# Performance work log

Hardware: AMD Instinct MI355X
Metric: run time of the kernel (lower is better)

Reference implementation:

```python
import jax, jax.numpy as jnp
import numpy as np

B, S, E, H, DH = 4, 2048, 1024, 16, 64  # batch, seq, embed, heads, head_dim


def setup_inputs() -> dict:
    key = jax.random.key(0)
    k0, k1, k2, k3 = jax.random.split(key, 4)
    scale = 1.0 / np.sqrt(E).astype(np.float32)
    embedded = jax.random.normal(k0, (B, S, E), jnp.float32)
    Wq = jax.random.normal(k1, (H, E, DH), jnp.float32) * scale
    Wk = jax.random.normal(k2, (H, E, DH), jnp.float32) * scale
    Wv = jax.random.normal(k3, (H, E, DH), jnp.float32) * scale
    return {"embedded": embedded, "Wq": Wq, "Wk": Wk, "Wv": Wv}


def reference(embedded, Wq, Wk, Wv):
    # Batched QKV projections across all heads (replaces per-head nn.Linear loop)
    q = jnp.einsum('bse,hed->bhsd', embedded, Wq)
    k = jnp.einsum('bse,hed->bhsd', embedded, Wk)
    v = jnp.einsum('bse,hed->bhsd', embedded, Wv)
    head_dim = q.shape[-1]
    scores = jnp.einsum('bhqd,bhkd->bhqk', q, k) / jnp.sqrt(jnp.asarray(head_dim, q.dtype))
    seq = scores.shape[-1]
    causal = jnp.tril(jnp.ones((seq, seq), dtype=bool))  # lower-triangular causal mask
    scores = jnp.where(causal, scores, jnp.finfo(scores.dtype).min)
    attn = jax.nn.softmax(scores, axis=-1)
    out = jnp.einsum('bhqk,bhkd->bhqd', attn, v)
    # concatenate heads along the feature dim (torch.cat(..., dim=2))
    b, h, s, d = out.shape
    return out.transpose(0, 2, 1, 3).reshape(b, s, h * d)
```

## Files before the change

### kernel.cpp

```cpp
#include <hip/hip_runtime.h>


typedef short bf16x4 __attribute__((ext_vector_type(4)));
typedef short bf16x8 __attribute__((ext_vector_type(8)));
typedef float f32x4 __attribute__((ext_vector_type(4)));
typedef unsigned short u16x4 __attribute__((ext_vector_type(4)));
typedef unsigned short u16x8 __attribute__((ext_vector_type(8)));

#define SCL 0.1803368801111204f

static __device__ __forceinline__ unsigned short f2bf(float f) {
  unsigned int u = __builtin_bit_cast(unsigned int, f);
  u += 0x7fffu + ((u >> 16) & 1u);
  return (unsigned short)(u >> 16);
}

static __device__ __forceinline__ void gload16(const void* g, void* l) {
  __builtin_amdgcn_global_load_lds((__attribute__((address_space(1))) void*)g,
                                   (__attribute__((address_space(3))) void*)l, 16, 0, 0);
}

__global__ __launch_bounds__(256) void conv_x(const float* __restrict__ x,
                                              unsigned short* __restrict__ y, int n4) {
  int i0 = blockIdx.x * 256 + threadIdx.x;
  int stride = gridDim.x * 256;
  for (int c = i0; c < n4; c += stride) {
    float4 v = ((const float4*)x)[c];
    u16x4 o;
    o[0] = f2bf(v.x); o[1] = f2bf(v.y); o[2] = f2bf(v.z); o[3] = f2bf(v.w);
    ((u16x4*)y)[c] = o;
  }
}

__global__ __launch_bounds__(256) void conv_w(const float* __restrict__ Wq,
                                              const float* __restrict__ Wk,
                                              const float* __restrict__ Wv,
                                              unsigned short* __restrict__ Wt) {
  const int p = blockIdx.y;
  const float* Wsrc = (p == 0) ? Wq : ((p == 1) ? Wk : Wv);
  const int h = blockIdx.x >> 4, et = blockIdx.x & 15;
  const int t = threadIdx.x;
  __shared__ __align__(16) unsigned short tile[64][72];

  const float* src = Wsrc + (h * 1024 + et * 64) * 64;
#pragma unroll
  for (int i = 0; i < 4; ++i) {
    int c = i * 256 + t;
    int r = c >> 4, cc = (c & 15) * 4;
    float4 v = *(const float4*)(src + r * 64 + cc);
    tile[r][cc + 0] = f2bf(v.x); tile[r][cc + 1] = f2bf(v.y);
    tile[r][cc + 2] = f2bf(v.z); tile[r][cc + 3] = f2bf(v.w);
  }
  __syncthreads();
#pragma unroll
  for (int i = 0; i < 2; ++i) {
    int c = i * 256 + t;
    int d = c >> 3, ec = (c & 7) * 8;
    u16x8 o;
#pragma unroll
    for (int j = 0; j < 8; ++j) o[j] = tile[ec + j][d];
    *(u16x8*)(Wt + (p * 1024 + h * 64 + d) * 1024 + et * 64 + ec) = o;
  }
}

__global__ __launch_bounds__(512, 2) void qkv_gemm(const unsigned short* __restrict__ Xb,
                                                   const unsigned short* __restrict__ Wt,
                                                   unsigned short* __restrict__ Qb,
                                                   unsigned short* __restrict__ Kb,
                                                   unsigned short* __restrict__ Vtb) {
  __shared__ __align__(16) unsigned short L[3][2][256 * 32];

  const int t = threadIdx.x, lane = t & 63, w = t >> 6;
  const int wr = w >> 2, wc = w & 3, c16 = lane & 15, g = lane >> 4;

  const int bid = blockIdx.x;
  const int xcd = bid & 7, l = bid >> 3;
  const int nt = l >> 2;
  const int m0 = (xcd * 4 + (l & 3)) * 256;
  const int p = nt >> 2;
  const int nb0 = (nt & 3) * 256;

  f32x4 acc[8][4] = {};

  const int srow = t >> 2;
  const int scl = (t & 3) ^ ((srow & 3) ^ ((srow >> 2) & 3));
  const int chp = (g ^ ((c16 & 3) ^ ((c16 >> 2) & 3))) * 8;

#define STAGE(KT, AB, HALF, BUF)                                                   \
  {                                                                                \
    const unsigned short* s_ =                                                     \
        (((AB) == 0) ? (Xb + (m0 + (HALF)*128) * 1024)                             \
                     : (Wt + (p * 1024 + nb0 + (HALF)*128) * 1024)) +              \
        (KT)*32 + srow * 1024 + scl * 8;                                           \
    gload16(s_, &L[BUF][AB][(HALF)*4096 + w * 512]);                               \
  }
#define LDA(BUF, MI) (*(const bf16x8*)&L[BUF][0][(wr * 128 + (MI)*16 + c16) * 32 + chp])
#define LDB(BUF, NI) (*(const bf16x8*)&L[BUF][1][(wc * 64 + (NI)*16 + c16) * 32 + chp])

  STAGE(0, 0, 0, 0); STAGE(0, 0, 1, 0); STAGE(0, 1, 0, 0); STAGE(0, 1, 1, 0);
  STAGE(1, 0, 0, 1); STAGE(1, 0, 1, 1); STAGE(1, 1, 0, 1); STAGE(1, 1, 1, 1);

  int buf = 0;
#pragma unroll 1
  for (int kt = 0; kt < 32; ++kt) {
    const int sbuf = (buf == 0) ? 2 : buf - 1;
    if (kt < 31) { asm volatile("s_waitcnt vmcnt(4)" ::: "memory"); }
    else         { asm volatile("s_waitcnt vmcnt(0)" ::: "memory"); }
    __builtin_amdgcn_s_barrier();

    bf16x8 bq[4], aq[4];
#pragma unroll
    for (int ni = 0; ni < 4; ++ni) bq[ni] = LDB(buf, ni);
#pragma unroll
    for (int mi = 0; mi < 4; ++mi) aq[mi] = LDA(buf, mi);
    if (kt < 30) { STAGE(kt + 2, 0, 0, sbuf); STAGE(kt + 2, 0, 1, sbuf); }
    asm volatile("s_waitcnt lgkmcnt(0)" ::: "memory");
    __builtin_amdgcn_sched_barrier(0);
    __builtin_amdgcn_s_setprio(1);
    if (p != 2) {
#pragma unroll
      for (int q = 0; q < 4; ++q)
#pragma unroll
        for (int ni = 0; ni < 4; ++ni)
          acc[q][ni] = __builtin_amdgcn_mfma_f32_16x16x32_bf16(aq[q], bq[ni], acc[q][ni], 0, 0, 0);
    } else {
#pragma unroll
      for (int q = 0; q < 4; ++q)
#pragma unroll
        for (int ni = 0; ni < 4; ++ni)
          acc[q][ni] = __builtin_amdgcn_mfma_f32_16x16x32_bf16(bq[ni], aq[q], acc[q][ni], 0, 0, 0);
    }
    __builtin_amdgcn_s_setprio(0);

    bf16x8 aq2[4];
#pragma unroll
    for (int mi = 0; mi < 4; ++mi) aq2[mi] = LDA(buf, 4 + mi);
    if (kt < 30) { STAGE(kt + 2, 1, 0, sbuf); STAGE(kt + 2, 1, 1, sbuf); }
    asm volatile("s_waitcnt lgkmcnt(0)" ::: "memory");
    __builtin_amdgcn_sched_barrier(0);
    __builtin_amdgcn_s_setprio(1);
    if (p != 2) {
#pragma unroll
      for (int q = 0; q < 4; ++q)
#pragma unroll
        for (int ni = 0; ni < 4; ++ni)
          acc[4 + q][ni] = __builtin_amdgcn_mfma_f32_16x16x32_bf16(aq2[q], bq[ni], acc[4 + q][ni], 0, 0, 0);
    } else {
#pragma unroll
      for (int q = 0; q < 4; ++q)
#pragma unroll
        for (int ni = 0; ni < 4; ++ni)
          acc[4 + q][ni] = __builtin_amdgcn_mfma_f32_16x16x32_bf16(bq[ni], aq2[q], acc[4 + q][ni], 0, 0, 0);
    }
    __builtin_amdgcn_s_setprio(0);

    buf = (buf == 2) ? 0 : buf + 1;
  }

  if (p != 2) {
    unsigned short* dst = (p == 0) ? Qb : Kb;
#pragma unroll
    for (int mi = 0; mi < 8; ++mi)
#pragma unroll
      for (int ni = 0; ni < 4; ++ni)
#pragma unroll
        for (int r = 0; r < 4; ++r) {
          int m_g = m0 + wr * 128 + mi * 16 + g * 4 + r;
          int n_g = nb0 + wc * 64 + ni * 16 + c16;
          int b = m_g >> 11, s = m_g & 2047;
          dst[((b * 16 + (n_g >> 6)) * 2048 + s) * 64 + (n_g & 63)] = f2bf(acc[mi][ni][r]);
        }
  } else {
#pragma unroll
    for (int mi = 0; mi < 8; ++mi)
#pragma unroll
      for (int ni = 0; ni < 4; ++ni)
#pragma unroll
        for (int r = 0; r < 4; ++r) {
          int n_g = nb0 + wc * 64 + ni * 16 + g * 4 + r;
          int m_g = m0 + wr * 128 + mi * 16 + c16;
          int b = m_g >> 11, s = m_g & 2047;
          Vtb[((b * 16 + (n_g >> 6)) * 64 + (n_g & 63)) * 2048 + s] = f2bf(acc[mi][ni][r]);
        }
  }
#undef STAGE
#undef LDA
#undef LDB
}

__global__ __launch_bounds__(256) void attn(const unsigned short* __restrict__ Qb,
                                            const unsigned short* __restrict__ Kb,
                                            const unsigned short* __restrict__ Vtb,
                                            float* __restrict__ out) {
  const int bid = blockIdx.x;
  const int xcd = bid & 7, slot = bid >> 3;
  const int bh = xcd * 8 + (slot >> 3);
  const int pp = slot & 7;
  const int b = bh >> 4, h = bh & 15;
  const int t = threadIdx.x, lane = t & 63, w = t >> 6;
  const int g = lane >> 4, c = lane & 15;

  __shared__ __align__(16) unsigned short Ks[2][64][72];
  __shared__ __align__(16) unsigned short Vs[2][64][72];

  for (int job = 0; job < 2; ++job) {
    const int qt = job ? pp : 15 - pp;
    const int q0 = qt * 128;
    const int ktiles = 2 * qt + 2;

    bf16x8 qf[2][2];
#pragma unroll
    for (int mi = 0; mi < 2; ++mi)
#pragma unroll
      for (int kc = 0; kc < 2; ++kc)
        qf[mi][kc] = *(const bf16x8*)(Qb + ((bh * 2048 + q0 + w * 32 + mi * 16 + c) << 6)
                                         + kc * 32 + g * 8);

    f32x4 o_acc[2][4] = {};
    float m_r[2] = {-INFINITY, -INFINITY};
    float l_r[2] = {0.f, 0.f};

    uint4 kr[2], vr[2];
#pragma unroll
    for (int i = 0; i < 2; ++i) {
      int cid = i * 256 + t;
      kr[i] = *(const uint4*)(Kb + ((bh * 2048) << 6) + cid * 8);
      vr[i] = *(const uint4*)(Vtb + ((bh * 64 + (cid >> 3)) << 11) + (cid & 7) * 8);
    }
#pragma unroll
    for (int i = 0; i < 2; ++i) {
      int cid = i * 256 + t;
      *(uint4*)&Ks[0][cid >> 3][(cid & 7) * 8] = kr[i];
      *(uint4*)&Vs[0][cid >> 3][(cid & 7) * 8] = vr[i];
    }
    __syncthreads();

    for (int kt = 0; kt < ktiles; ++kt) {
      const int cur = kt & 1;
      if (kt + 1 < ktiles) {
        const int kv0n = (kt + 1) * 64;
#pragma unroll
        for (int i = 0; i < 2; ++i) {
          int cid = i * 256 + t;
          kr[i] = *(const uint4*)(Kb + ((bh * 2048 + kv0n) << 6) + cid * 8);
          vr[i] = *(const uint4*)(Vtb + ((bh * 64 + (cid >> 3)) << 11) + kv0n + (cid & 7) * 8);
        }
      }

      f32x4 sc[2][4];
#pragma unroll
      for (int sub = 0; sub < 4; ++sub) {
        bf16x8 kf0 = *(const bf16x8*)&Ks[cur][sub * 16 + c][g * 8];
        bf16x8 kf1 = *(const bf16x8*)&Ks[cur][sub * 16 + c][32 + g * 8];
#pragma unroll
        for (int mi = 0; mi < 2; ++mi) {
          f32x4 z = {};
          z = __builtin_amdgcn_mfma_f32_16x16x32_bf16(kf0, qf[mi][0], z, 0, 0, 0);
          z = __builtin_amdgcn_mfma_f32_16x16x32_bf16(kf1, qf[mi][1], z, 0, 0, 0);
          sc[mi][sub] = z;
        }
      }

      if (kt >= 2 * qt) {
        const int koff = (kt - 2 * qt) * 64;
#pragma unroll
        for (int mi = 0; mi < 2; ++mi) {
          const int q_l = w * 32 + mi * 16 + c;
#pragma unroll
          for (int sub = 0; sub < 4; ++sub)
#pragma unroll
            for (int r = 0; r < 4; ++r)
              if (koff + sub * 16 + 4 * g + r > q_l) sc[mi][sub][r] = -INFINITY;
        }
      }

      float mx[2];
#pragma unroll
      for (int mi = 0; mi < 2; ++mi) {
        float v0 = fmaxf(fmaxf(sc[mi][0][0], sc[mi][0][1]), fmaxf(sc[mi][0][2], sc[mi][0][3]));
        float v1 = fmaxf(fmaxf(sc[mi][1][0], sc[mi][1][1]), fmaxf(sc[mi][1][2], sc[mi][1][3]));
        float v2 = fmaxf(fmaxf(sc[mi][2][0], sc[mi][2][1]), fmaxf(sc[mi][2][2], sc[mi][2][3]));
        float v3 = fmaxf(fmaxf(sc[mi][3][0], sc[mi][3][1]), fmaxf(sc[mi][3][2], sc[mi][3][3]));
        float v = fmaxf(fmaxf(v0, v1), fmaxf(v2, v3));
        v = fmaxf(v, __shfl_xor(v, 16));
        v = fmaxf(v, __shfl_xor(v, 32));
        mx[mi] = v;
      }

      bool need = (mx[0] > m_r[0] + 44.f) || (mx[1] > m_r[1] + 44.f);
      if (__any(need)) {
#pragma unroll
        for (int mi = 0; mi < 2; ++mi) {
          float mnew = fmaxf(m_r[mi], mx[mi]);
          float corr = __builtin_amdgcn_exp2f((m_r[mi] - mnew) * SCL);
          m_r[mi] = mnew;
          l_r[mi] *= corr;
#pragma unroll
          for (int ni = 0; ni < 4; ++ni) o_acc[mi][ni] *= corr;
        }
      }

      bf16x8 pb[2][2];
#pragma unroll
      for (int mi = 0; mi < 2; ++mi) {
        const float a = -m_r[mi] * SCL;
        float s = 0.f;
#pragma unroll
        for (int sub = 0; sub < 4; ++sub)
#pragma unroll
          for (int r = 0; r < 4; ++r) {
            float e = __builtin_amdgcn_exp2f(fmaf(sc[mi][sub][r], SCL, a));
            sc[mi][sub][r] = e;
            s += e;
          }
        s += __shfl_xor(s, 16);
        s += __shfl_xor(s, 32);
        l_r[mi] += s;
#pragma unroll
        for (int j = 0; j < 8; ++j) {
          pb[mi][0][j] = (short)f2bf(sc[mi][j >> 2][j & 3]);
          pb[mi][1][j] = (short)f2bf(sc[mi][2 + (j >> 2)][j & 3]);
        }
      }

#pragma unroll
      for (int ni = 0; ni < 4; ++ni)
#pragma unroll
        for (int half = 0; half < 2; ++half) {
          bf16x4 lo = *(const bf16x4*)&Vs[cur][ni * 16 + c][half * 32 + 4 * g];
          bf16x4 hi = *(const bf16x4*)&Vs[cur][ni * 16 + c][half * 32 + 16 + 4 * g];
          bf16x8 vt = __builtin_shufflevector(lo, hi, 0, 1, 2, 3, 4, 5, 6, 7);
#pragma unroll
          for (int mi = 0; mi < 2; ++mi)
            o_acc[mi][ni] = __builtin_amdgcn_mfma_f32_16x16x32_bf16(vt, pb[mi][half],
                                                                    o_acc[mi][ni], 0, 0, 0);
        }

      if (kt + 1 < ktiles) {
#pragma unroll
        for (int i = 0; i < 2; ++i) {
          int cid = i * 256 + t;
          *(uint4*)&Ks[cur ^ 1][cid >> 3][(cid & 7) * 8] = kr[i];
          *(uint4*)&Vs[cur ^ 1][cid >> 3][(cid & 7) * 8] = vr[i];
        }
      }
      __syncthreads();
    }

#pragma unroll
    for (int mi = 0; mi < 2; ++mi) {
      const float inv = 1.f / l_r[mi];
      const int q_g = q0 + w * 32 + mi * 16 + c;
      float* orow = out + (b * 2048 + q_g) * 1024 + h * 64;
#pragma unroll
      for (int ni = 0; ni < 4; ++ni) {
        f32x4 o = o_acc[mi][ni] * inv;
        *(f32x4*)(orow + ni * 16 + 4 * g) = o;
      }
    }
  }
}

extern "C" void kernel_launch(void* const* d_in, const int* in_sizes, int n_in,
                              void* d_out, int out_size, void* d_ws, size_t ws_size,
                              hipStream_t stream) {
  const float* emb = (const float*)d_in[0];
  const float* Wq  = (const float*)d_in[1];
  const float* Wk  = (const float*)d_in[2];
  const float* Wv  = (const float*)d_in[3];
  char* ws = (char*)d_ws;
  unsigned short* Xb  = (unsigned short*)(ws + 0);
  unsigned short* Wt  = (unsigned short*)(ws + 16777216);
  unsigned short* Qb  = (unsigned short*)(ws + 23068672);
  unsigned short* Kb  = (unsigned short*)(ws + 39845888);
  unsigned short* Vtb = (unsigned short*)(ws + 56623104);
  float* out = (float*)d_out;

  conv_x<<<2048, 256, 0, stream>>>(emb, Xb, 2097152);
  conv_w<<<dim3(256, 3), 256, 0, stream>>>(Wq, Wk, Wv, Wt);
  qkv_gemm<<<384, 512, 0, stream>>>(Xb, Wt, Qb, Kb, Vtb);
  attn<<<512, 256, 0, stream>>>(Qb, Kb, Vtb, out);
}
```

Measured before the change: 178.5 us.

## Shrink QKV GEMM tiles to 256x128 with 256-thread blocks and 768-block grid

```diff
diff --git a/kernel.cpp b/kernel.cpp
--- a/kernel.cpp
+++ b/kernel.cpp
@@ -63,48 +63,57 @@
   }
 }
 
-__global__ __launch_bounds__(512, 2) void qkv_gemm(const unsigned short* __restrict__ Xb,
+__global__ __launch_bounds__(256, 2) void qkv_gemm(const unsigned short* __restrict__ Xb,
                                                    const unsigned short* __restrict__ Wt,
                                                    unsigned short* __restrict__ Qb,
                                                    unsigned short* __restrict__ Kb,
                                                    unsigned short* __restrict__ Vtb) {
-  __shared__ __align__(16) unsigned short L[3][2][256 * 32];
+  __shared__ __align__(16) unsigned short L[3][12288];
 
   const int t = threadIdx.x, lane = t & 63, w = t >> 6;
-  const int wr = w >> 2, wc = w & 3, c16 = lane & 15, g = lane >> 4;
+  const int wr = w >> 1, wc = w & 1, c16 = lane & 15, g = lane >> 4;
 
   const int bid = blockIdx.x;
   const int xcd = bid & 7, l = bid >> 3;
   const int nt = l >> 2;
   const int m0 = (xcd * 4 + (l & 3)) * 256;
-  const int p = nt >> 2;
-  const int nb0 = (nt & 3) * 256;
+  const int p = nt >> 3;
+  const int nb0 = (nt & 7) * 128;
 
   f32x4 acc[8][4] = {};
 
-  const int srow = t >> 2;
-  const int scl = (t & 3) ^ ((srow & 3) ^ ((srow >> 2) & 3));
+  const int ar0 = t >> 2,           as0 = (t & 3) ^ ((ar0 & 3) ^ ((ar0 >> 2) & 3));
+  const int ar1 = (256 + t) >> 2,   as1 = ((256 + t) & 3) ^ ((ar1 & 3) ^ ((ar1 >> 2) & 3));
+  const int ar2 = (512 + t) >> 2,   as2 = ((512 + t) & 3) ^ ((ar2 & 3) ^ ((ar2 >> 2) & 3));
+  const int ar3 = (768 + t) >> 2,   as3 = ((768 + t) & 3) ^ ((ar3 & 3) ^ ((ar3 >> 2) & 3));
   const int chp = (g ^ ((c16 & 3) ^ ((c16 >> 2) & 3))) * 8;
 
-#define STAGE(KT, AB, HALF, BUF)                                                   \
-  {                                                                                \
-    const unsigned short* s_ =                                                     \
-        (((AB) == 0) ? (Xb + (m0 + (HALF)*128) * 1024)                             \
-                     : (Wt + (p * 1024 + nb0 + (HALF)*128) * 1024)) +              \
-        (KT)*32 + srow * 1024 + scl * 8;                                           \
-    gload16(s_, &L[BUF][AB][(HALF)*4096 + w * 512]);                               \
-  }
-#define LDA(BUF, MI) (*(const bf16x8*)&L[BUF][0][(wr * 128 + (MI)*16 + c16) * 32 + chp])
-#define LDB(BUF, NI) (*(const bf16x8*)&L[BUF][1][(wc * 64 + (NI)*16 + c16) * 32 + chp])
-
-  STAGE(0, 0, 0, 0); STAGE(0, 0, 1, 0); STAGE(0, 1, 0, 0); STAGE(0, 1, 1, 0);
-  STAGE(1, 0, 0, 1); STAGE(1, 0, 1, 1); STAGE(1, 1, 0, 1); STAGE(1, 1, 1, 1);
+  const unsigned short* Abase = Xb + m0 * 1024;
+  const unsigned short* Bbase = Wt + (p * 1024 + nb0) * 1024;
+
+#define STAGE_A(KT, BUF)                                                          \
+  {                                                                               \
+    gload16(Abase + ar0 * 1024 + (KT)*32 + as0 * 8, &L[BUF][(0 * 256 + w * 64) * 8]); \
+    gload16(Abase + ar1 * 1024 + (KT)*32 + as1 * 8, &L[BUF][(1 * 256 + w * 64) * 8]); \
+    gload16(Abase + ar2 * 1024 + (KT)*32 + as2 * 8, &L[BUF][(2 * 256 + w * 64) * 8]); \
+    gload16(Abase + ar3 * 1024 + (KT)*32 + as3 * 8, &L[BUF][(3 * 256 + w * 64) * 8]); \
+  }
+#define STAGE_B(KT, BUF)                                                          \
+  {                                                                               \
+    gload16(Bbase + ar0 * 1024 + (KT)*32 + as0 * 8, &L[BUF][8192 + (0 * 256 + w * 64) * 8]); \
+    gload16(Bbase + ar1 * 1024 + (KT)*32 + as1 * 8, &L[BUF][8192 + (1 * 256 + w * 64) * 8]); \
+  }
+#define LDA(BUF, MI) (*(const bf16x8*)&L[BUF][(wr * 128 + (MI)*16 + c16) * 32 + chp])
+#define LDB(BUF, NI) (*(const bf16x8*)&L[BUF][8192 + (wc * 64 + (NI)*16 + c16) * 32 + chp])
+
+  STAGE_A(0, 0); STAGE_B(0, 0);
+  STAGE_A(1, 1); STAGE_B(1, 1);
 
   int buf = 0;
 #pragma unroll 1
   for (int kt = 0; kt < 32; ++kt) {
     const int sbuf = (buf == 0) ? 2 : buf - 1;
-    if (kt < 31) { asm volatile("s_waitcnt vmcnt(4)" ::: "memory"); }
+    if (kt < 31) { asm volatile("s_waitcnt vmcnt(6)" ::: "memory"); }
     else         { asm volatile("s_waitcnt vmcnt(0)" ::: "memory"); }
     __builtin_amdgcn_s_barrier();
 
@@ -113,7 +122,7 @@
     for (int ni = 0; ni < 4; ++ni) bq[ni] = LDB(buf, ni);
 #pragma unroll
     for (int mi = 0; mi < 4; ++mi) aq[mi] = LDA(buf, mi);
-    if (kt < 30) { STAGE(kt + 2, 0, 0, sbuf); STAGE(kt + 2, 0, 1, sbuf); }
+    if (kt < 30) STAGE_A(kt + 2, sbuf);
     asm volatile("s_waitcnt lgkmcnt(0)" ::: "memory");
     __builtin_amdgcn_sched_barrier(0);
     __builtin_amdgcn_s_setprio(1);
@@ -135,7 +144,7 @@
     bf16x8 aq2[4];
 #pragma unroll
     for (int mi = 0; mi < 4; ++mi) aq2[mi] = LDA(buf, 4 + mi);
-    if (kt < 30) { STAGE(kt + 2, 1, 0, sbuf); STAGE(kt + 2, 1, 1, sbuf); }
+    if (kt < 30) STAGE_B(kt + 2, sbuf);
     asm volatile("s_waitcnt lgkmcnt(0)" ::: "memory");
     __builtin_amdgcn_sched_barrier(0);
     __builtin_amdgcn_s_setprio(1);
@@ -183,7 +192,8 @@
           Vtb[((b * 16 + (n_g >> 6)) * 64 + (n_g & 63)) * 2048 + s] = f2bf(acc[mi][ni][r]);
         }
   }
-#undef STAGE
+#undef STAGE_A
+#undef STAGE_B
 #undef LDA
 #undef LDB
 }
@@ -378,6 +388,6 @@
 
   conv_x<<<2048, 256, 0, stream>>>(emb, Xb, 2097152);
   conv_w<<<dim3(256, 3), 256, 0, stream>>>(Wq, Wk, Wv, Wt);
-  qkv_gemm<<<384, 512, 0, stream>>>(Xb, Wt, Qb, Kb, Vtb);
+  qkv_gemm<<<768, 256, 0, stream>>>(Xb, Wt, Qb, Kb, Vtb);
   attn<<<512, 256, 0, stream>>>(Qb, Kb, Vtb, out);
 }
```

Result: slower. 211.0 us (+18.2%).
